# Optimization experiments

Hardware: AMD Instinct MI355X
Metric: run time of the kernel (lower is better)

## Reference

```python
import jax, jax.numpy as jnp
import numpy as np

B, DIN, DOUT, NW = 32768, 768, 768, 48
NH = NW // 3  # num_haar == num_mexican == num_morlet == 16 for NW=48
OMEGA0 = 5.0
LN_EPS = 1e-5


def setup_inputs() -> dict:
    key = jax.random.key(0)
    ks = jax.random.split(key, 6)
    x = jax.random.normal(ks[0], (B, DIN), dtype=jnp.float32)
    # kaiming-normal-ish fan_in init for linear layers, zero bias
    W = jax.random.normal(ks[1], (DOUT, DIN), dtype=jnp.float32) / np.sqrt(DIN)
    b = jnp.zeros((DOUT,), jnp.float32)
    Wp = jax.random.normal(ks[2], (NW, DIN), dtype=jnp.float32) / np.sqrt(DIN)
    bp = jnp.zeros((NW,), jnp.float32)
    Wc = jax.random.normal(ks[3], (DOUT, NW), dtype=jnp.float32) / np.sqrt(NW)
    bc = jnp.zeros((DOUT,), jnp.float32)
    # mixed-type init: per-family logspace scales / linspace translations
    scales = jnp.asarray(np.concatenate([
        np.logspace(-0.5, 0.5, NH),
        np.logspace(-0.3, 0.7, NH),
        np.logspace(-0.3, 0.7, NW - 2 * NH)]), jnp.float32)
    translations = jnp.asarray(np.concatenate([
        np.linspace(-1.5, 1.5, NH),
        np.linspace(-1.5, 1.5, NH),
        np.linspace(-1.5, 1.5, NW - 2 * NH)]), jnp.float32)
    gamma = jnp.ones((DOUT,), jnp.float32)
    beta = jnp.zeros((DOUT,), jnp.float32)
    return {"x": x, "W": W, "b": b, "Wp": Wp, "bp": bp, "Wc": Wc,
            "bc": bc, "scales": scales, "translations": translations,
            "gamma": gamma, "beta": beta}


def _wavelet_basis(s):
    # s: [B, NW] already scaled/translated; columns split by family
    dt = s.dtype
    sh = s[:, :NH]
    haar = (((sh >= 0) & (sh < 0.5)).astype(dt)
            - ((sh >= 0.5) & (sh < 1.0)).astype(dt))
    sm = s[:, NH:2 * NH]
    mexican = (1.0 - sm * sm) * jnp.exp(-0.5 * sm * sm)
    so = s[:, 2 * NH:]
    morlet = jnp.cos(OMEGA0 * so) * jnp.exp(-0.5 * so * so)
    return jnp.concatenate([haar, mexican, morlet], axis=1)


def reference(x, W, b, Wp, bp, Wc, bc, scales, translations, gamma, beta):
    direct = x @ W.T + b                              # [B, DOUT]
    wi = x @ Wp.T + bp                                # [B, NW]
    s = (wi - translations) / scales                  # [B, NW]
    wav = jax.nn.gelu(_wavelet_basis(s), approximate=False)
    wpath = wav @ Wc.T + bc                           # [B, DOUT]
    h = direct + wpath
    mu = jnp.mean(h, axis=-1, keepdims=True)
    var = jnp.mean((h - mu) ** 2, axis=-1, keepdims=True)
    return (h - mu) * jax.lax.rsqrt(var + LN_EPS) * gamma + beta
```

## Files before the change

### kernel.cpp

```cpp
#include <hip/hip_runtime.h>
#include <math.h>


#define B_SZ  32768
#define DIN   768
#define DOUT  768
#define NWAV  48

#define WF_OFF   0
#define WPH_OFF  589824
#define WPL_OFF  638976
#define WCF_OFF  688128

typedef short bf16x8 __attribute__((ext_vector_type(8)));
typedef float f32x16 __attribute__((ext_vector_type(16)));

__device__ __forceinline__ float bf2f(short u) {
    union { unsigned int i; float f; } v;
    v.i = ((unsigned int)(unsigned short)u) << 16;
    return v.f;
}
__device__ __forceinline__ short f2bf(float f) {
    union { float f; unsigned int i; } v; v.f = f;
    unsigned int r = v.i + 0x7FFFu + ((v.i >> 16) & 1u);
    return (short)(r >> 16);
}

__global__ __launch_bounds__(256) void pack_kernel(
    const float* __restrict__ W, const float* __restrict__ Wp,
    const float* __restrict__ Wc, short* __restrict__ ws)
{
    const int gw = (blockIdx.x * 256 + threadIdx.x) >> 6;
    const int L  = threadIdx.x & 63;
    const int lm = L & 31, half = L >> 5;

    if (gw < 1152) {
        const int cb = gw / 48, kb = gw % 48;
        const int row = cb * 32 + lm;
        const int k = kb * 16 + half * 8;
        bf16x8 o;
#pragma unroll
        for (int j = 0; j < 8; j++) o[j] = f2bf(W[(size_t)row * DIN + k + j]);
        *reinterpret_cast<bf16x8*>(&ws[WF_OFF + (size_t)gw * 512 + L * 8]) = o;
    } else if (gw < 1248) {
        const int t = gw - 1152;
        const int ct = t / 48, kb = t % 48;
        const int j = ct * 32 + lm;
        const int k = kb * 16 + half * 8;
        bf16x8 h, l;
#pragma unroll
        for (int jj = 0; jj < 8; jj++) {
            float v = (j < NWAV) ? Wp[(size_t)j * DIN + k + jj] : 0.f;
            const short hh = f2bf(v);
            h[jj] = hh;
            l[jj] = f2bf(v - bf2f(hh));
        }
        *reinterpret_cast<bf16x8*>(&ws[WPH_OFF + (size_t)t * 512 + L * 8]) = h;
        *reinterpret_cast<bf16x8*>(&ws[WPL_OFF + (size_t)t * 512 + L * 8]) = l;
    } else if (gw < 1320) {
        const int t = gw - 1248;
        const int cb = t / 3, kb = t % 3;
        const int row = cb * 32 + lm;
        const int k = kb * 16 + half * 8;
        bf16x8 o;
#pragma unroll
        for (int jj = 0; jj < 8; jj++) o[jj] = f2bf(Wc[(size_t)row * NWAV + k + jj]);
        *reinterpret_cast<bf16x8*>(&ws[WCF_OFF + (size_t)t * 512 + L * 8]) = o;
    }
}

__global__ __launch_bounds__(512, 2) void fused_kernel(
    const float* __restrict__ x, const short* __restrict__ ws,
    const float* __restrict__ Wp,
    const float* __restrict__ bp, const float* __restrict__ sc,
    const float* __restrict__ tr,
    const float* __restrict__ bb, const float* __restrict__ bc,
    const float* __restrict__ gm, const float* __restrict__ bt,
    float* __restrict__ out)
{
    __shared__ __align__(16) short xh[4][64 * 72];
    __shared__ __align__(16) short xl[4][64 * 72];
    __shared__ float redS[64 * 8], redQ[64 * 8];
    __shared__ float muA[64], rsA[64];
    __shared__ unsigned flags[64];
    __shared__ double dred[8];

    const short* WF  = ws + WF_OFF;
    const short* WPH = ws + WPH_OFF;
    const short* WPL = ws + WPL_OFF;
    const short* WCF = ws + WCF_OFF;

    const int tid = threadIdx.x;
    const int r0  = blockIdx.x * 64;
    const int L   = tid & 63;
    const int wv  = __builtin_amdgcn_readfirstlane(tid >> 6);
    const int lm  = L & 31, half = L >> 5;
    const int L8  = L * 8;
    const bool wi = (wv < 4);
    const int wv3 = wv * 3;
    const int wrt = wv & 1, wct = wv >> 1;
    const int wct48 = wct * 48;

    if (tid < 64) flags[tid] = 0u;

    f32x16 acc[2][3];
#pragma unroll
    for (int rt = 0; rt < 2; rt++)
#pragma unroll
        for (int ct = 0; ct < 3; ct++)
#pragma unroll
            for (int g = 0; g < 16; g++) acc[rt][ct][g] = 0.f;
    f32x16 wacc;
#pragma unroll
    for (int g = 0; g < 16; g++) wacc[g] = 0.f;

    const int srow = tid >> 3;
    const int sk   = (tid & 7) * 8;

#pragma unroll
    for (int c = 0; c < 2; ++c) {
        const float4* xp = reinterpret_cast<const float4*>(
            &x[(size_t)(r0 + srow) * DIN + c * 64 + sk]);
        const float4 v0 = xp[0], v1 = xp[1];
        const float f[8] = {v0.x, v0.y, v0.z, v0.w, v1.x, v1.y, v1.z, v1.w};
        bf16x8 hh, ll;
#pragma unroll
        for (int i = 0; i < 8; i++) {
            const short h = f2bf(f[i]);
            hh[i] = h;
            ll[i] = f2bf(f[i] - bf2f(h));
        }
        *reinterpret_cast<bf16x8*>(&xh[c][srow * 72 + sk]) = hh;
        *reinterpret_cast<bf16x8*>(&xl[c][srow * 72 + sk]) = ll;
    }
    __syncthreads();

    for (int s = 0; s < 6; ++s) {
        const int kA = 2 * s, kB = 2 * s + 1;
        const int bA = kA & 3, bB = kB & 3;
        const int kbA = kA * 4, kbB = kB * 4;

        bf16x8 bfrA[4][3];
#pragma unroll
        for (int ks = 0; ks < 4; ++ks)
#pragma unroll
            for (int ct = 0; ct < 3; ++ct)
                bfrA[ks][ct] = *reinterpret_cast<const bf16x8*>(
                    &WF[((size_t)((wv3 + ct) * 48 + kbA + ks)) * 512 + L8]);
        bf16x8 bwhA[4], bwlA[4];
        if (wi) {
#pragma unroll
            for (int ks = 0; ks < 4; ++ks) {
                bwhA[ks] = *reinterpret_cast<const bf16x8*>(
                    &WPH[((size_t)(wct48 + kbA + ks)) * 512 + L8]);
                bwlA[ks] = *reinterpret_cast<const bf16x8*>(
                    &WPL[((size_t)(wct48 + kbA + ks)) * 512 + L8]);
            }
        }
        float4 vA0, vA1;
        if (s < 5) {
            const float4* xp = reinterpret_cast<const float4*>(
                &x[(size_t)(r0 + srow) * DIN + (kA + 2) * 64 + sk]);
            vA0 = xp[0]; vA1 = xp[1];
        }

#pragma unroll
        for (int ks = 0; ks < 4; ++ks) {
            const bf16x8 a0 = *reinterpret_cast<bf16x8*>(
                &xh[bA][lm * 72 + ks * 16 + half * 8]);
            const bf16x8 a1 = *reinterpret_cast<bf16x8*>(
                &xh[bA][(32 + lm) * 72 + ks * 16 + half * 8]);
#pragma unroll
            for (int ct = 0; ct < 3; ++ct) {
                acc[0][ct] = __builtin_amdgcn_mfma_f32_32x32x16_bf16(a0, bfrA[ks][ct], acc[0][ct], 0, 0, 0);
                acc[1][ct] = __builtin_amdgcn_mfma_f32_32x32x16_bf16(a1, bfrA[ks][ct], acc[1][ct], 0, 0, 0);
            }
            if (wi) {
                const bf16x8 ah = wrt ? a1 : a0;
                const bf16x8 al = *reinterpret_cast<bf16x8*>(
                    &xl[bA][(wrt * 32 + lm) * 72 + ks * 16 + half * 8]);
                wacc = __builtin_amdgcn_mfma_f32_32x32x16_bf16(ah, bwlA[ks], wacc, 0, 0, 0);
                wacc = __builtin_amdgcn_mfma_f32_32x32x16_bf16(al, bwhA[ks], wacc, 0, 0, 0);
                wacc = __builtin_amdgcn_mfma_f32_32x32x16_bf16(ah, bwhA[ks], wacc, 0, 0, 0);
            }
        }

        bf16x8 bfrB[4][3];
#pragma unroll
        for (int ks = 0; ks < 4; ++ks)
#pragma unroll
            for (int ct = 0; ct < 3; ++ct)
                bfrB[ks][ct] = *reinterpret_cast<const bf16x8*>(
                    &WF[((size_t)((wv3 + ct) * 48 + kbB + ks)) * 512 + L8]);
        bf16x8 bwhB[4], bwlB[4];
        if (wi) {
#pragma unroll
            for (int ks = 0; ks < 4; ++ks) {
                bwhB[ks] = *reinterpret_cast<const bf16x8*>(
                    &WPH[((size_t)(wct48 + kbB + ks)) * 512 + L8]);
                bwlB[ks] = *reinterpret_cast<const bf16x8*>(
                    &WPL[((size_t)(wct48 + kbB + ks)) * 512 + L8]);
            }
        }
        float4 vB0, vB1;
        if (s < 5) {
            const float4* xp = reinterpret_cast<const float4*>(
                &x[(size_t)(r0 + srow) * DIN + (kB + 2) * 64 + sk]);
            vB0 = xp[0]; vB1 = xp[1];
        }

#pragma unroll
        for (int ks = 0; ks < 4; ++ks) {
            const bf16x8 a0 = *reinterpret_cast<bf16x8*>(
                &xh[bB][lm * 72 + ks * 16 + half * 8]);
            const bf16x8 a1 = *reinterpret_cast<bf16x8*>(
                &xh[bB][(32 + lm) * 72 + ks * 16 + half * 8]);
#pragma unroll
            for (int ct = 0; ct < 3; ++ct) {
                acc[0][ct] = __builtin_amdgcn_mfma_f32_32x32x16_bf16(a0, bfrB[ks][ct], acc[0][ct], 0, 0, 0);
                acc[1][ct] = __builtin_amdgcn_mfma_f32_32x32x16_bf16(a1, bfrB[ks][ct], acc[1][ct], 0, 0, 0);
            }
            if (wi) {
                const bf16x8 ah = wrt ? a1 : a0;
                const bf16x8 al = *reinterpret_cast<bf16x8*>(
                    &xl[bB][(wrt * 32 + lm) * 72 + ks * 16 + half * 8]);
                wacc = __builtin_amdgcn_mfma_f32_32x32x16_bf16(ah, bwlB[ks], wacc, 0, 0, 0);
                wacc = __builtin_amdgcn_mfma_f32_32x32x16_bf16(al, bwhB[ks], wacc, 0, 0, 0);
                wacc = __builtin_amdgcn_mfma_f32_32x32x16_bf16(ah, bwhB[ks], wacc, 0, 0, 0);
            }
        }

        if (s < 5) {
            {
                const float f[8] = {vA0.x, vA0.y, vA0.z, vA0.w, vA1.x, vA1.y, vA1.z, vA1.w};
                bf16x8 hh, ll;
#pragma unroll
                for (int i = 0; i < 8; i++) {
                    const short h = f2bf(f[i]);
                    hh[i] = h;
                    ll[i] = f2bf(f[i] - bf2f(h));
                }
                const int bn = (kA + 2) & 3;
                *reinterpret_cast<bf16x8*>(&xh[bn][srow * 72 + sk]) = hh;
                *reinterpret_cast<bf16x8*>(&xl[bn][srow * 72 + sk]) = ll;
            }
            {
                const float f[8] = {vB0.x, vB0.y, vB0.z, vB0.w, vB1.x, vB1.y, vB1.z, vB1.w};
                bf16x8 hh, ll;
#pragma unroll
                for (int i = 0; i < 8; i++) {
                    const short h = f2bf(f[i]);
                    hh[i] = h;
                    ll[i] = f2bf(f[i] - bf2f(h));
                }
                const int bn = (kB + 2) & 3;
                *reinterpret_cast<bf16x8*>(&xh[bn][srow * 72 + sk]) = hh;
                *reinterpret_cast<bf16x8*>(&xl[bn][srow * 72 + sk]) = ll;
            }
        }
        __syncthreads();
    }

    short* wavL = &xh[0][0];
    if (wi) {
        const int j = wct * 32 + lm;
        if (j < NWAV) {
            const float bpv = bp[j], scv = sc[j], trv = tr[j];
#pragma unroll
            for (int g = 0; g < 16; ++g) {
                const int rowl = wrt * 32 + (g & 3) + 8 * (g >> 2) + 4 * half;
                const float wiv = wacc[g] + bpv;
                const float s = (wiv - trv) / scv;
                float w;
                if (j < 16) {
                    const float dmin = fminf(fabsf(s), fminf(fabsf(s - 0.5f), fabsf(s - 1.0f)));
                    if (dmin < 2e-4f) atomicOr(&flags[rowl], 1u << j);
                    w = (s >= 0.f && s < 0.5f) ? 1.f : ((s >= 0.5f && s < 1.f) ? -1.f : 0.f);
                } else if (j < 32) {
                    w = (1.f - s * s) * expf(-0.5f * s * s);
                } else {
                    w = cosf(5.f * s) * expf(-0.5f * s * s);
                }
                const float gel = 0.5f * w * (1.f + erff(w * 0.70710678118654752f));
                wavL[rowl * 72 + j] = f2bf(gel);
            }
        }
    }
    __syncthreads();

#pragma unroll 1
    for (int fr = 0; fr < 64; ++fr) {
        unsigned m = flags[fr];
        while (m) {
            const int j = __ffs(m) - 1;
            m &= m - 1;
            const float* xr = &x[(size_t)(r0 + fr) * DIN];
            const float* wr = &Wp[(size_t)j * DIN];
            double a = (double)xr[tid] * (double)wr[tid];
            if (tid < DIN - 512)
                a += (double)xr[tid + 512] * (double)wr[tid + 512];
            a += __shfl_xor(a, 1);  a += __shfl_xor(a, 2);
            a += __shfl_xor(a, 4);  a += __shfl_xor(a, 8);
            a += __shfl_xor(a, 16); a += __shfl_xor(a, 32);
            if (L == 0) dred[wv] = a;
            __syncthreads();
            if (tid == 0) {
                double wid = (double)bp[j];
#pragma unroll
                for (int i = 0; i < 8; i++) wid += dred[i];
                const double sd = (wid - (double)tr[j]) / (double)sc[j];
                const double w = (sd >= 0.0 && sd < 0.5) ? 1.0
                               : ((sd >= 0.5 && sd < 1.0) ? -1.0 : 0.0);
                const double gel = 0.5 * w * (1.0 + erf(w * 0.70710678118654752));
                wavL[fr * 72 + j] = f2bf((float)gel);
            }
            __syncthreads();
        }
    }

#pragma unroll
    for (int ks = 0; ks < 3; ++ks) {
        const bf16x8 a0 = *reinterpret_cast<bf16x8*>(&wavL[lm * 72 + ks * 16 + half * 8]);
        const bf16x8 a1 = *reinterpret_cast<bf16x8*>(&wavL[(32 + lm) * 72 + ks * 16 + half * 8]);
#pragma unroll
        for (int ct = 0; ct < 3; ++ct) {
            const bf16x8 b = *reinterpret_cast<const bf16x8*>(
                &WCF[((size_t)((wv3 + ct) * 3 + ks)) * 512 + L8]);
            acc[0][ct] = __builtin_amdgcn_mfma_f32_32x32x16_bf16(a0, b, acc[0][ct], 0, 0, 0);
            acc[1][ct] = __builtin_amdgcn_mfma_f32_32x32x16_bf16(a1, b, acc[1][ct], 0, 0, 0);
        }
    }

    float bias[3], gmv[3], btv[3];
#pragma unroll
    for (int ct = 0; ct < 3; ++ct) {
        const int col = wv * 96 + ct * 32 + lm;
        bias[ct] = bb[col] + bc[col];
        gmv[ct] = gm[col];
        btv[ct] = bt[col];
    }
#pragma unroll
    for (int rt = 0; rt < 2; ++rt) {
#pragma unroll
        for (int g = 0; g < 16; ++g) {
            const float v0 = acc[rt][0][g] + bias[0];
            const float v1 = acc[rt][1][g] + bias[1];
            const float v2 = acc[rt][2][g] + bias[2];
            acc[rt][0][g] = v0; acc[rt][1][g] = v1; acc[rt][2][g] = v2;
            float s1 = v0 + v1 + v2;
            float s2 = v0 * v0 + v1 * v1 + v2 * v2;
            s1 += __shfl_xor(s1, 1);  s2 += __shfl_xor(s2, 1);
            s1 += __shfl_xor(s1, 2);  s2 += __shfl_xor(s2, 2);
            s1 += __shfl_xor(s1, 4);  s2 += __shfl_xor(s2, 4);
            s1 += __shfl_xor(s1, 8);  s2 += __shfl_xor(s2, 8);
            s1 += __shfl_xor(s1, 16); s2 += __shfl_xor(s2, 16);
            if (lm == 0) {
                const int rowl = rt * 32 + (g & 3) + 8 * (g >> 2) + 4 * half;
                redS[rowl * 8 + wv] = s1;
                redQ[rowl * 8 + wv] = s2;
            }
        }
    }
    __syncthreads();
    if (tid < 64) {
        float S = 0.f, Q = 0.f;
#pragma unroll
        for (int i = 0; i < 8; i++) { S += redS[tid * 8 + i]; Q += redQ[tid * 8 + i]; }
        const float mu = S * (1.f / 768.f);
        const float var = Q * (1.f / 768.f) - mu * mu;
        muA[tid] = mu;
        rsA[tid] = rsqrtf(var + 1e-5f);
    }
    __syncthreads();

#pragma unroll
    for (int rt = 0; rt < 2; ++rt) {
#pragma unroll
        for (int g = 0; g < 16; ++g) {
            const int rowl = rt * 32 + (g & 3) + 8 * (g >> 2) + 4 * half;
            const float mu = muA[rowl], rs = rsA[rowl];
            float* orow = &out[(size_t)(r0 + rowl) * DOUT + wv * 96 + lm];
#pragma unroll
            for (int ct = 0; ct < 3; ++ct) {
                orow[ct * 32] = (acc[rt][ct][g] - mu) * rs * gmv[ct] + btv[ct];
            }
        }
    }
}

extern "C" void kernel_launch(void* const* d_in, const int* in_sizes, int n_in,
                              void* d_out, int out_size, void* d_ws, size_t ws_size,
                              hipStream_t stream)
{
    const float* x  = (const float*)d_in[0];
    const float* W  = (const float*)d_in[1];
    const float* b  = (const float*)d_in[2];
    const float* Wp = (const float*)d_in[3];
    const float* bp = (const float*)d_in[4];
    const float* Wc = (const float*)d_in[5];
    const float* bc = (const float*)d_in[6];
    const float* sc = (const float*)d_in[7];
    const float* tr = (const float*)d_in[8];
    const float* gm = (const float*)d_in[9];
    const float* bt = (const float*)d_in[10];
    float* out = (float*)d_out;
    short* ws  = (short*)d_ws;

    pack_kernel<<<dim3(330), dim3(256), 0, stream>>>(W, Wp, Wc, ws);
    fused_kernel<<<dim3(B_SZ / 64), dim3(512), 0, stream>>>(
        x, ws, Wp, bp, sc, tr, b, bc, gm, bt, out);
}
```

Measured before the change: 265.9 us.

## Fuse weight packing into persistent main kernel with grid-wide barrier

Drops the separate pack kernel. The 256 blocks of the main kernel now pack the bf16 weight tiles themselves and wait on a global atomic-counter barrier before starting, and each block then handles two row tiles. The aim is to remove the second kernel launch and the serialization between the two kernels. The trade-offs are a hipMemsetAsync on every call, a spin barrier that deadlocks unless all 256 blocks are co-resident, and half as many blocks as before, which may reduce latency hiding.

```diff
diff --git a/kernel.cpp b/kernel.cpp
--- a/kernel.cpp
+++ b/kernel.cpp
@@ -11,6 +11,7 @@
 #define WPH_OFF  589824
 #define WPL_OFF  638976
 #define WCF_OFF  688128
+#define CTR_OFF  724992
 
 typedef short bf16x8 __attribute__((ext_vector_type(8)));
 typedef float f32x16 __attribute__((ext_vector_type(16)));
@@ -26,52 +27,10 @@
     return (short)(r >> 16);
 }
 
-__global__ __launch_bounds__(256) void pack_kernel(
-    const float* __restrict__ W, const float* __restrict__ Wp,
-    const float* __restrict__ Wc, short* __restrict__ ws)
-{
-    const int gw = (blockIdx.x * 256 + threadIdx.x) >> 6;
-    const int L  = threadIdx.x & 63;
-    const int lm = L & 31, half = L >> 5;
-
-    if (gw < 1152) {
-        const int cb = gw / 48, kb = gw % 48;
-        const int row = cb * 32 + lm;
-        const int k = kb * 16 + half * 8;
-        bf16x8 o;
-#pragma unroll
-        for (int j = 0; j < 8; j++) o[j] = f2bf(W[(size_t)row * DIN + k + j]);
-        *reinterpret_cast<bf16x8*>(&ws[WF_OFF + (size_t)gw * 512 + L * 8]) = o;
-    } else if (gw < 1248) {
-        const int t = gw - 1152;
-        const int ct = t / 48, kb = t % 48;
-        const int j = ct * 32 + lm;
-        const int k = kb * 16 + half * 8;
-        bf16x8 h, l;
-#pragma unroll
-        for (int jj = 0; jj < 8; jj++) {
-            float v = (j < NWAV) ? Wp[(size_t)j * DIN + k + jj] : 0.f;
-            const short hh = f2bf(v);
-            h[jj] = hh;
-            l[jj] = f2bf(v - bf2f(hh));
-        }
-        *reinterpret_cast<bf16x8*>(&ws[WPH_OFF + (size_t)t * 512 + L * 8]) = h;
-        *reinterpret_cast<bf16x8*>(&ws[WPL_OFF + (size_t)t * 512 + L * 8]) = l;
-    } else if (gw < 1320) {
-        const int t = gw - 1248;
-        const int cb = t / 3, kb = t % 3;
-        const int row = cb * 32 + lm;
-        const int k = kb * 16 + half * 8;
-        bf16x8 o;
-#pragma unroll
-        for (int jj = 0; jj < 8; jj++) o[jj] = f2bf(Wc[(size_t)row * NWAV + k + jj]);
-        *reinterpret_cast<bf16x8*>(&ws[WCF_OFF + (size_t)t * 512 + L * 8]) = o;
-    }
-}
-
 __global__ __launch_bounds__(512, 2) void fused_kernel(
-    const float* __restrict__ x, const short* __restrict__ ws,
-    const float* __restrict__ Wp,
+    const float* __restrict__ x,  const float* __restrict__ W,
+    const float* __restrict__ Wp, const float* __restrict__ Wc,
+    short* __restrict__ ws,
     const float* __restrict__ bp, const float* __restrict__ sc,
     const float* __restrict__ tr,
     const float* __restrict__ bb, const float* __restrict__ bc,
@@ -85,13 +44,7 @@
     __shared__ unsigned flags[64];
     __shared__ double dred[8];
 
-    const short* WF  = ws + WF_OFF;
-    const short* WPH = ws + WPH_OFF;
-    const short* WPL = ws + WPL_OFF;
-    const short* WCF = ws + WCF_OFF;
-
     const int tid = threadIdx.x;
-    const int r0  = blockIdx.x * 64;
     const int L   = tid & 63;
     const int wv  = __builtin_amdgcn_readfirstlane(tid >> 6);
     const int lm  = L & 31, half = L >> 5;
@@ -101,288 +54,347 @@
     const int wrt = wv & 1, wct = wv >> 1;
     const int wct48 = wct * 48;
 
-    if (tid < 64) flags[tid] = 0u;
-
-    f32x16 acc[2][3];
-#pragma unroll
-    for (int rt = 0; rt < 2; rt++)
-#pragma unroll
-        for (int ct = 0; ct < 3; ct++)
-#pragma unroll
-            for (int g = 0; g < 16; g++) acc[rt][ct][g] = 0.f;
-    f32x16 wacc;
-#pragma unroll
-    for (int g = 0; g < 16; g++) wacc[g] = 0.f;
+    {
+        const int gw = blockIdx.x * 8 + wv;
+        if (gw < 1152) {
+            const int cb = gw / 48, kb = gw % 48;
+            const int row = cb * 32 + lm;
+            const int k = kb * 16 + half * 8;
+            bf16x8 o;
+#pragma unroll
+            for (int j = 0; j < 8; j++) o[j] = f2bf(W[(size_t)row * DIN + k + j]);
+            *reinterpret_cast<bf16x8*>(&ws[WF_OFF + (size_t)gw * 512 + L8]) = o;
+        } else if (gw < 1248) {
+            const int t = gw - 1152;
+            const int ct = t / 48, kb = t % 48;
+            const int j = ct * 32 + lm;
+            const int k = kb * 16 + half * 8;
+            bf16x8 h, l;
+#pragma unroll
+            for (int jj = 0; jj < 8; jj++) {
+                float v = (j < NWAV) ? Wp[(size_t)j * DIN + k + jj] : 0.f;
+                const short hh = f2bf(v);
+                h[jj] = hh;
+                l[jj] = f2bf(v - bf2f(hh));
+            }
+            *reinterpret_cast<bf16x8*>(&ws[WPH_OFF + (size_t)t * 512 + L8]) = h;
+            *reinterpret_cast<bf16x8*>(&ws[WPL_OFF + (size_t)t * 512 + L8]) = l;
+        } else if (gw < 1320) {
+            const int t = gw - 1248;
+            const int cb = t / 3, kb = t % 3;
+            const int row = cb * 32 + lm;
+            const int k = kb * 16 + half * 8;
+            bf16x8 o;
+#pragma unroll
+            for (int jj = 0; jj < 8; jj++) o[jj] = f2bf(Wc[(size_t)row * NWAV + k + jj]);
+            *reinterpret_cast<bf16x8*>(&ws[WCF_OFF + (size_t)t * 512 + L8]) = o;
+        }
+    }
+
+    {
+        unsigned* ctr = reinterpret_cast<unsigned*>(ws + CTR_OFF);
+        __syncthreads();
+        if (tid == 0) {
+            __threadfence();
+            atomicAdd(ctr, 1u);
+            while (atomicAdd(ctr, 0u) < 256u) { }
+            __threadfence();
+        }
+        __syncthreads();
+    }
+
+    const short* WF  = ws + WF_OFF;
+    const short* WPH = ws + WPH_OFF;
+    const short* WPL = ws + WPL_OFF;
+    const short* WCF = ws + WCF_OFF;
 
     const int srow = tid >> 3;
     const int sk   = (tid & 7) * 8;
 
-#pragma unroll
-    for (int c = 0; c < 2; ++c) {
-        const float4* xp = reinterpret_cast<const float4*>(
-            &x[(size_t)(r0 + srow) * DIN + c * 64 + sk]);
-        const float4 v0 = xp[0], v1 = xp[1];
-        const float f[8] = {v0.x, v0.y, v0.z, v0.w, v1.x, v1.y, v1.z, v1.w};
-        bf16x8 hh, ll;
-#pragma unroll
-        for (int i = 0; i < 8; i++) {
-            const short h = f2bf(f[i]);
-            hh[i] = h;
-            ll[i] = f2bf(f[i] - bf2f(h));
-        }
-        *reinterpret_cast<bf16x8*>(&xh[c][srow * 72 + sk]) = hh;
-        *reinterpret_cast<bf16x8*>(&xl[c][srow * 72 + sk]) = ll;
-    }
-    __syncthreads();
-
-    for (int s = 0; s < 6; ++s) {
-        const int kA = 2 * s, kB = 2 * s + 1;
-        const int bA = kA & 3, bB = kB & 3;
-        const int kbA = kA * 4, kbB = kB * 4;
-
-        bf16x8 bfrA[4][3];
-#pragma unroll
-        for (int ks = 0; ks < 4; ++ks)
-#pragma unroll
-            for (int ct = 0; ct < 3; ++ct)
-                bfrA[ks][ct] = *reinterpret_cast<const bf16x8*>(
-                    &WF[((size_t)((wv3 + ct) * 48 + kbA + ks)) * 512 + L8]);
-        bf16x8 bwhA[4], bwlA[4];
+#pragma unroll 1
+    for (int pass = 0; pass < 2; ++pass) {
+        const int r0 = (blockIdx.x + (pass << 8)) * 64;
+
+        if (tid < 64) flags[tid] = 0u;
+
+        f32x16 acc[2][3];
+#pragma unroll
+        for (int rt = 0; rt < 2; rt++)
+#pragma unroll
+            for (int ct = 0; ct < 3; ct++)
+#pragma unroll
+                for (int g = 0; g < 16; g++) acc[rt][ct][g] = 0.f;
+        f32x16 wacc;
+#pragma unroll
+        for (int g = 0; g < 16; g++) wacc[g] = 0.f;
+
+#pragma unroll
+        for (int c = 0; c < 2; ++c) {
+            const float4* xp = reinterpret_cast<const float4*>(
+                &x[(size_t)(r0 + srow) * DIN + c * 64 + sk]);
+            const float4 v0 = xp[0], v1 = xp[1];
+            const float f[8] = {v0.x, v0.y, v0.z, v0.w, v1.x, v1.y, v1.z, v1.w};
+            bf16x8 hh, ll;
+#pragma unroll
+            for (int i = 0; i < 8; i++) {
+                const short h = f2bf(f[i]);
+                hh[i] = h;
+                ll[i] = f2bf(f[i] - bf2f(h));
+            }
+            *reinterpret_cast<bf16x8*>(&xh[c][srow * 72 + sk]) = hh;
+            *reinterpret_cast<bf16x8*>(&xl[c][srow * 72 + sk]) = ll;
+        }
+        __syncthreads();
+
+        for (int s = 0; s < 6; ++s) {
+            const int kA = 2 * s, kB = 2 * s + 1;
+            const int bA = kA & 3, bB = kB & 3;
+            const int kbA = kA * 4, kbB = kB * 4;
+
+            bf16x8 bfrA[4][3];
+#pragma unroll
+            for (int ks = 0; ks < 4; ++ks)
+#pragma unroll
+                for (int ct = 0; ct < 3; ++ct)
+                    bfrA[ks][ct] = *reinterpret_cast<const bf16x8*>(
+                        &WF[((size_t)((wv3 + ct) * 48 + kbA + ks)) * 512 + L8]);
+            bf16x8 bwhA[4], bwlA[4];
+            if (wi) {
+#pragma unroll
+                for (int ks = 0; ks < 4; ++ks) {
+                    bwhA[ks] = *reinterpret_cast<const bf16x8*>(
+                        &WPH[((size_t)(wct48 + kbA + ks)) * 512 + L8]);
+                    bwlA[ks] = *reinterpret_cast<const bf16x8*>(
+                        &WPL[((size_t)(wct48 + kbA + ks)) * 512 + L8]);
+                }
+            }
+            float4 vA0, vA1;
+            if (s < 5) {
+                const float4* xp = reinterpret_cast<const float4*>(
+                    &x[(size_t)(r0 + srow) * DIN + (kA + 2) * 64 + sk]);
+                vA0 = xp[0]; vA1 = xp[1];
+            }
+
+#pragma unroll
+            for (int ks = 0; ks < 4; ++ks) {
+                const bf16x8 a0 = *reinterpret_cast<bf16x8*>(
+                    &xh[bA][lm * 72 + ks * 16 + half * 8]);
+                const bf16x8 a1 = *reinterpret_cast<bf16x8*>(
+                    &xh[bA][(32 + lm) * 72 + ks * 16 + half * 8]);
+#pragma unroll
+                for (int ct = 0; ct < 3; ++ct) {
+                    acc[0][ct] = __builtin_amdgcn_mfma_f32_32x32x16_bf16(a0, bfrA[ks][ct], acc[0][ct], 0, 0, 0);
+                    acc[1][ct] = __builtin_amdgcn_mfma_f32_32x32x16_bf16(a1, bfrA[ks][ct], acc[1][ct], 0, 0, 0);
+                }
+                if (wi) {
+                    const bf16x8 ah = wrt ? a1 : a0;
+                    const bf16x8 al = *reinterpret_cast<bf16x8*>(
+                        &xl[bA][(wrt * 32 + lm) * 72 + ks * 16 + half * 8]);
+                    wacc = __builtin_amdgcn_mfma_f32_32x32x16_bf16(ah, bwlA[ks], wacc, 0, 0, 0);
+                    wacc = __builtin_amdgcn_mfma_f32_32x32x16_bf16(al, bwhA[ks], wacc, 0, 0, 0);
+                    wacc = __builtin_amdgcn_mfma_f32_32x32x16_bf16(ah, bwhA[ks], wacc, 0, 0, 0);
+                }
+            }
+
+            bf16x8 bfrB[4][3];
+#pragma unroll
+            for (int ks = 0; ks < 4; ++ks)
+#pragma unroll
+                for (int ct = 0; ct < 3; ++ct)
+                    bfrB[ks][ct] = *reinterpret_cast<const bf16x8*>(
+                        &WF[((size_t)((wv3 + ct) * 48 + kbB + ks)) * 512 + L8]);
+            bf16x8 bwhB[4], bwlB[4];
+            if (wi) {
+#pragma unroll
+                for (int ks = 0; ks < 4; ++ks) {
+                    bwhB[ks] = *reinterpret_cast<const bf16x8*>(
+                        &WPH[((size_t)(wct48 + kbB + ks)) * 512 + L8]);
+                    bwlB[ks] = *reinterpret_cast<const bf16x8*>(
+                        &WPL[((size_t)(wct48 + kbB + ks)) * 512 + L8]);
+                }
+            }
+            float4 vB0, vB1;
+            if (s < 5) {
+                const float4* xp = reinterpret_cast<const float4*>(
+                    &x[(size_t)(r0 + srow) * DIN + (kB + 2) * 64 + sk]);
+                vB0 = xp[0]; vB1 = xp[1];
+            }
+
+#pragma unroll
+            for (int ks = 0; ks < 4; ++ks) {
+                const bf16x8 a0 = *reinterpret_cast<bf16x8*>(
+                    &xh[bB][lm * 72 + ks * 16 + half * 8]);
+                const bf16x8 a1 = *reinterpret_cast<bf16x8*>(
+                    &xh[bB][(32 + lm) * 72 + ks * 16 + half * 8]);
+#pragma unroll
+                for (int ct = 0; ct < 3; ++ct) {
+                    acc[0][ct] = __builtin_amdgcn_mfma_f32_32x32x16_bf16(a0, bfrB[ks][ct], acc[0][ct], 0, 0, 0);
+                    acc[1][ct] = __builtin_amdgcn_mfma_f32_32x32x16_bf16(a1, bfrB[ks][ct], acc[1][ct], 0, 0, 0);
+                }
+                if (wi) {
+                    const bf16x8 ah = wrt ? a1 : a0;
+                    const bf16x8 al = *reinterpret_cast<bf16x8*>(
+                        &xl[bB][(wrt * 32 + lm) * 72 + ks * 16 + half * 8]);
+                    wacc = __builtin_amdgcn_mfma_f32_32x32x16_bf16(ah, bwlB[ks], wacc, 0, 0, 0);
+                    wacc = __builtin_amdgcn_mfma_f32_32x32x16_bf16(al, bwhB[ks], wacc, 0, 0, 0);
+                    wacc = __builtin_amdgcn_mfma_f32_32x32x16_bf16(ah, bwhB[ks], wacc, 0, 0, 0);
+                }
+            }
+
+            if (s < 5) {
+                {
+                    const float f[8] = {vA0.x, vA0.y, vA0.z, vA0.w, vA1.x, vA1.y, vA1.z, vA1.w};
+                    bf16x8 hh, ll;
+#pragma unroll
+                    for (int i = 0; i < 8; i++) {
+                        const short h = f2bf(f[i]);
+                        hh[i] = h;
+                        ll[i] = f2bf(f[i] - bf2f(h));
+                    }
+                    const int bn = (kA + 2) & 3;
+                    *reinterpret_cast<bf16x8*>(&xh[bn][srow * 72 + sk]) = hh;
+                    *reinterpret_cast<bf16x8*>(&xl[bn][srow * 72 + sk]) = ll;
+                }
+                {
+                    const float f[8] = {vB0.x, vB0.y, vB0.z, vB0.w, vB1.x, vB1.y, vB1.z, vB1.w};
+                    bf16x8 hh, ll;
+#pragma unroll
+                    for (int i = 0; i < 8; i++) {
+                        const short h = f2bf(f[i]);
+                        hh[i] = h;
+                        ll[i] = f2bf(f[i] - bf2f(h));
+                    }
+                    const int bn = (kB + 2) & 3;
+                    *reinterpret_cast<bf16x8*>(&xh[bn][srow * 72 + sk]) = hh;
+                    *reinterpret_cast<bf16x8*>(&xl[bn][srow * 72 + sk]) = ll;
+                }
+            }
+            __syncthreads();
+        }
+
+        short* wavL = &xh[0][0];
         if (wi) {
-#pragma unroll
-            for (int ks = 0; ks < 4; ++ks) {
-                bwhA[ks] = *reinterpret_cast<const bf16x8*>(
-                    &WPH[((size_t)(wct48 + kbA + ks)) * 512 + L8]);
-                bwlA[ks] = *reinterpret_cast<const bf16x8*>(
-                    &WPL[((size_t)(wct48 + kbA + ks)) * 512 + L8]);
-            }
-        }
-        float4 vA0, vA1;
-        if (s < 5) {
-            const float4* xp = reinterpret_cast<const float4*>(
-                &x[(size_t)(r0 + srow) * DIN + (kA + 2) * 64 + sk]);
-            vA0 = xp[0]; vA1 = xp[1];
-        }
-
-#pragma unroll
-        for (int ks = 0; ks < 4; ++ks) {
-            const bf16x8 a0 = *reinterpret_cast<bf16x8*>(
-                &xh[bA][lm * 72 + ks * 16 + half * 8]);
-            const bf16x8 a1 = *reinterpret_cast<bf16x8*>(
-                &xh[bA][(32 + lm) * 72 + ks * 16 + half * 8]);
+            const int j = wct * 32 + lm;
+            if (j < NWAV) {
+                const float bpv = bp[j], scv = sc[j], trv = tr[j];
+#pragma unroll
+                for (int g = 0; g < 16; ++g) {
+                    const int rowl = wrt * 32 + (g & 3) + 8 * (g >> 2) + 4 * half;
+                    const float wiv = wacc[g] + bpv;
+                    const float s = (wiv - trv) / scv;
+                    float w;
+                    if (j < 16) {
+                        const float dmin = fminf(fabsf(s), fminf(fabsf(s - 0.5f), fabsf(s - 1.0f)));
+                        if (dmin < 2e-4f) atomicOr(&flags[rowl], 1u << j);
+                        w = (s >= 0.f && s < 0.5f) ? 1.f : ((s >= 0.5f && s < 1.f) ? -1.f : 0.f);
+                    } else if (j < 32) {
+                        w = (1.f - s * s) * expf(-0.5f * s * s);
+                    } else {
+                        w = cosf(5.f * s) * expf(-0.5f * s * s);
+                    }
+                    const float gel = 0.5f * w * (1.f + erff(w * 0.70710678118654752f));
+                    wavL[rowl * 72 + j] = f2bf(gel);
+                }
+            }
+        }
+        __syncthreads();
+
+#pragma unroll 1
+        for (int fr = 0; fr < 64; ++fr) {
+            unsigned m = flags[fr];
+            while (m) {
+                const int j = __ffs(m) - 1;
+                m &= m - 1;
+                const float* xr = &x[(size_t)(r0 + fr) * DIN];
+                const float* wr = &Wp[(size_t)j * DIN];
+                double a = (double)xr[tid] * (double)wr[tid];
+                if (tid < DIN - 512)
+                    a += (double)xr[tid + 512] * (double)wr[tid + 512];
+                a += __shfl_xor(a, 1);  a += __shfl_xor(a, 2);
+                a += __shfl_xor(a, 4);  a += __shfl_xor(a, 8);
+                a += __shfl_xor(a, 16); a += __shfl_xor(a, 32);
+                if (L == 0) dred[wv] = a;
+                __syncthreads();
+                if (tid == 0) {
+                    double wid = (double)bp[j];
+#pragma unroll
+                    for (int i = 0; i < 8; i++) wid += dred[i];
+                    const double sd = (wid - (double)tr[j]) / (double)sc[j];
+                    const double w = (sd >= 0.0 && sd < 0.5) ? 1.0
+                                   : ((sd >= 0.5 && sd < 1.0) ? -1.0 : 0.0);
+                    const double gel = 0.5 * w * (1.0 + erf(w * 0.70710678118654752));
+                    wavL[fr * 72 + j] = f2bf((float)gel);
+                }
+                __syncthreads();
+            }
+        }
+
+#pragma unroll
+        for (int ks = 0; ks < 3; ++ks) {
+            const bf16x8 a0 = *reinterpret_cast<bf16x8*>(&wavL[lm * 72 + ks * 16 + half * 8]);
+            const bf16x8 a1 = *reinterpret_cast<bf16x8*>(&wavL[(32 + lm) * 72 + ks * 16 + half * 8]);
 #pragma unroll
             for (int ct = 0; ct < 3; ++ct) {
-                acc[0][ct] = __builtin_amdgcn_mfma_f32_32x32x16_bf16(a0, bfrA[ks][ct], acc[0][ct], 0, 0, 0);
-                acc[1][ct] = __builtin_amdgcn_mfma_f32_32x32x16_bf16(a1, bfrA[ks][ct], acc[1][ct], 0, 0, 0);
-            }
-            if (wi) {
-                const bf16x8 ah = wrt ? a1 : a0;
-                const bf16x8 al = *reinterpret_cast<bf16x8*>(
-                    &xl[bA][(wrt * 32 + lm) * 72 + ks * 16 + half * 8]);
-                wacc = __builtin_amdgcn_mfma_f32_32x32x16_bf16(ah, bwlA[ks], wacc, 0, 0, 0);
-                wacc = __builtin_amdgcn_mfma_f32_32x32x16_bf16(al, bwhA[ks], wacc, 0, 0, 0);
-                wacc = __builtin_amdgcn_mfma_f32_32x32x16_bf16(ah, bwhA[ks], wacc, 0, 0, 0);
-            }
-        }
-
-        bf16x8 bfrB[4][3];
-#pragma unroll
-        for (int ks = 0; ks < 4; ++ks)
-#pragma unroll
-            for (int ct = 0; ct < 3; ++ct)
-                bfrB[ks][ct] = *reinterpret_cast<const bf16x8*>(
-                    &WF[((size_t)((wv3 + ct) * 48 + kbB + ks)) * 512 + L8]);
-        bf16x8 bwhB[4], bwlB[4];
-        if (wi) {
-#pragma unroll
-            for (int ks = 0; ks < 4; ++ks) {
-                bwhB[ks] = *reinterpret_cast<const bf16x8*>(
-                    &WPH[((size_t)(wct48 + kbB + ks)) * 512 + L8]);
-                bwlB[ks] = *reinterpret_cast<const bf16x8*>(
-                    &WPL[((size_t)(wct48 + kbB + ks)) * 512 + L8]);
-            }
-        }
-        float4 vB0, vB1;
-        if (s < 5) {
-            const float4* xp = reinterpret_cast<const float4*>(
-                &x[(size_t)(r0 + srow) * DIN + (kB + 2) * 64 + sk]);
-            vB0 = xp[0]; vB1 = xp[1];
-        }
-
-#pragma unroll
-        for (int ks = 0; ks < 4; ++ks) {
-            const bf16x8 a0 = *reinterpret_cast<bf16x8*>(
-                &xh[bB][lm * 72 + ks * 16 + half * 8]);
-            const bf16x8 a1 = *reinterpret_cast<bf16x8*>(
-                &xh[bB][(32 + lm) * 72 + ks * 16 + half * 8]);
-#pragma unroll
-            for (int ct = 0; ct < 3; ++ct) {
-                acc[0][ct] = __builtin_amdgcn_mfma_f32_32x32x16_bf16(a0, bfrB[ks][ct], acc[0][ct], 0, 0, 0);
-                acc[1][ct] = __builtin_amdgcn_mfma_f32_32x32x16_bf16(a1, bfrB[ks][ct], acc[1][ct], 0, 0, 0);
-            }
-            if (wi) {
-                const bf16x8 ah = wrt ? a1 : a0;
-                const bf16x8 al = *reinterpret_cast<bf16x8*>(
-                    &xl[bB][(wrt * 32 + lm) * 72 + ks * 16 + half * 8]);
-                wacc = __builtin_amdgcn_mfma_f32_32x32x16_bf16(ah, bwlB[ks], wacc, 0, 0, 0);
-                wacc = __builtin_amdgcn_mfma_f32_32x32x16_bf16(al, bwhB[ks], wacc, 0, 0, 0);
-                wacc = __builtin_amdgcn_mfma_f32_32x32x16_bf16(ah, bwhB[ks], wacc, 0, 0, 0);
-            }
-        }
-
-        if (s < 5) {
-            {
-                const float f[8] = {vA0.x, vA0.y, vA0.z, vA0.w, vA1.x, vA1.y, vA1.z, vA1.w};
-                bf16x8 hh, ll;
-#pragma unroll
-                for (int i = 0; i < 8; i++) {
-                    const short h = f2bf(f[i]);
-                    hh[i] = h;
-                    ll[i] = f2bf(f[i] - bf2f(h));
-                }
-                const int bn = (kA + 2) & 3;
-                *reinterpret_cast<bf16x8*>(&xh[bn][srow * 72 + sk]) = hh;
-                *reinterpret_cast<bf16x8*>(&xl[bn][srow * 72 + sk]) = ll;
-            }
-            {
-                const float f[8] = {vB0.x, vB0.y, vB0.z, vB0.w, vB1.x, vB1.y, vB1.z, vB1.w};
-                bf16x8 hh, ll;
-#pragma unroll
-                for (int i = 0; i < 8; i++) {
-                    const short h = f2bf(f[i]);
-                    hh[i] = h;
-                    ll[i] = f2bf(f[i] - bf2f(h));
-                }
-                const int bn = (kB + 2) & 3;
-                *reinterpret_cast<bf16x8*>(&xh[bn][srow * 72 + sk]) = hh;
-                *reinterpret_cast<bf16x8*>(&xl[bn][srow * 72 + sk]) = ll;
-            }
-        }
-        __syncthreads();
-    }
-
-    short* wavL = &xh[0][0];
-    if (wi) {
-        const int j = wct * 32 + lm;
-        if (j < NWAV) {
-            const float bpv = bp[j], scv = sc[j], trv = tr[j];
+                const bf16x8 b = *reinterpret_cast<const bf16x8*>(
+                    &WCF[((size_t)((wv3 + ct) * 3 + ks)) * 512 + L8]);
+                acc[0][ct] = __builtin_amdgcn_mfma_f32_32x32x16_bf16(a0, b, acc[0][ct], 0, 0, 0);
+                acc[1][ct] = __builtin_amdgcn_mfma_f32_32x32x16_bf16(a1, b, acc[1][ct], 0, 0, 0);
+            }
+        }
+
+        float bias[3], gmv[3], btv[3];
+#pragma unroll
+        for (int ct = 0; ct < 3; ++ct) {
+            const int col = wv * 96 + ct * 32 + lm;
+            bias[ct] = bb[col] + bc[col];
+            gmv[ct] = gm[col];
+            btv[ct] = bt[col];
+        }
+#pragma unroll
+        for (int rt = 0; rt < 2; ++rt) {
 #pragma unroll
             for (int g = 0; g < 16; ++g) {
-                const int rowl = wrt * 32 + (g & 3) + 8 * (g >> 2) + 4 * half;
-                const float wiv = wacc[g] + bpv;
-                const float s = (wiv - trv) / scv;
-                float w;
-                if (j < 16) {
-                    const float dmin = fminf(fabsf(s), fminf(fabsf(s - 0.5f), fabsf(s - 1.0f)));
-                    if (dmin < 2e-4f) atomicOr(&flags[rowl], 1u << j);
-                    w = (s >= 0.f && s < 0.5f) ? 1.f : ((s >= 0.5f && s < 1.f) ? -1.f : 0.f);
-                } else if (j < 32) {
-                    w = (1.f - s * s) * expf(-0.5f * s * s);
-                } else {
-                    w = cosf(5.f * s) * expf(-0.5f * s * s);
-                }
-                const float gel = 0.5f * w * (1.f + erff(w * 0.70710678118654752f));
-                wavL[rowl * 72 + j] = f2bf(gel);
-            }
-        }
-    }
-    __syncthreads();
-
-#pragma unroll 1
-    for (int fr = 0; fr < 64; ++fr) {
-        unsigned m = flags[fr];
-        while (m) {
-            const int j = __ffs(m) - 1;
-            m &= m - 1;
-            const float* xr = &x[(size_t)(r0 + fr) * DIN];
-            const float* wr = &Wp[(size_t)j * DIN];
-            double a = (double)xr[tid] * (double)wr[tid];
-            if (tid < DIN - 512)
-                a += (double)xr[tid + 512] * (double)wr[tid + 512];
-            a += __shfl_xor(a, 1);  a += __shfl_xor(a, 2);
-            a += __shfl_xor(a, 4);  a += __shfl_xor(a, 8);
-            a += __shfl_xor(a, 16); a += __shfl_xor(a, 32);
-            if (L == 0) dred[wv] = a;
-            __syncthreads();
-            if (tid == 0) {
-                double wid = (double)bp[j];
-#pragma unroll
-                for (int i = 0; i < 8; i++) wid += dred[i];
-                const double sd = (wid - (double)tr[j]) / (double)sc[j];
-                const double w = (sd >= 0.0 && sd < 0.5) ? 1.0
-                               : ((sd >= 0.5 && sd < 1.0) ? -1.0 : 0.0);
-                const double gel = 0.5 * w * (1.0 + erf(w * 0.70710678118654752));
-                wavL[fr * 72 + j] = f2bf((float)gel);
-            }
-            __syncthreads();
-        }
-    }
-
-#pragma unroll
-    for (int ks = 0; ks < 3; ++ks) {
-        const bf16x8 a0 = *reinterpret_cast<bf16x8*>(&wavL[lm * 72 + ks * 16 + half * 8]);
-        const bf16x8 a1 = *reinterpret_cast<bf16x8*>(&wavL[(32 + lm) * 72 + ks * 16 + half * 8]);
-#pragma unroll
-        for (int ct = 0; ct < 3; ++ct) {
-            const bf16x8 b = *reinterpret_cast<const bf16x8*>(
-                &WCF[((size_t)((wv3 + ct) * 3 + ks)) * 512 + L8]);
-            acc[0][ct] = __builtin_amdgcn_mfma_f32_32x32x16_bf16(a0, b, acc[0][ct], 0, 0, 0);
-            acc[1][ct] = __builtin_amdgcn_mfma_f32_32x32x16_bf16(a1, b, acc[1][ct], 0, 0, 0);
-        }
-    }
-
-    float bias[3], gmv[3], btv[3];
-#pragma unroll
-    for (int ct = 0; ct < 3; ++ct) {
-        const int col = wv * 96 + ct * 32 + lm;
-        bias[ct] = bb[col] + bc[col];
-        gmv[ct] = gm[col];
-        btv[ct] = bt[col];
-    }
-#pragma unroll
-    for (int rt = 0; rt < 2; ++rt) {
-#pragma unroll
-        for (int g = 0; g < 16; ++g) {
-            const float v0 = acc[rt][0][g] + bias[0];
-            const float v1 = acc[rt][1][g] + bias[1];
-            const float v2 = acc[rt][2][g] + bias[2];
-            acc[rt][0][g] = v0; acc[rt][1][g] = v1; acc[rt][2][g] = v2;
-            float s1 = v0 + v1 + v2;
-            float s2 = v0 * v0 + v1 * v1 + v2 * v2;
-            s1 += __shfl_xor(s1, 1);  s2 += __shfl_xor(s2, 1);
-            s1 += __shfl_xor(s1, 2);  s2 += __shfl_xor(s2, 2);
-            s1 += __shfl_xor(s1, 4);  s2 += __shfl_xor(s2, 4);
-            s1 += __shfl_xor(s1, 8);  s2 += __shfl_xor(s2, 8);
-            s1 += __shfl_xor(s1, 16); s2 += __shfl_xor(s2, 16);
-            if (lm == 0) {
+                const float v0 = acc[rt][0][g] + bias[0];
+                const float v1 = acc[rt][1][g] + bias[1];
+                const float v2 = acc[rt][2][g] + bias[2];
+                acc[rt][0][g] = v0; acc[rt][1][g] = v1; acc[rt][2][g] = v2;
+                float s1 = v0 + v1 + v2;
+                float s2 = v0 * v0 + v1 * v1 + v2 * v2;
+                s1 += __shfl_xor(s1, 1);  s2 += __shfl_xor(s2, 1);
+                s1 += __shfl_xor(s1, 2);  s2 += __shfl_xor(s2, 2);
+                s1 += __shfl_xor(s1, 4);  s2 += __shfl_xor(s2, 4);
+                s1 += __shfl_xor(s1, 8);  s2 += __shfl_xor(s2, 8);
+                s1 += __shfl_xor(s1, 16); s2 += __shfl_xor(s2, 16);
+                if (lm == 0) {
+                    const int rowl = rt * 32 + (g & 3) + 8 * (g >> 2) + 4 * half;
+                    redS[rowl * 8 + wv] = s1;
+                    redQ[rowl * 8 + wv] = s2;
+                }
+            }
+        }
+        __syncthreads();
+        if (tid < 64) {
+            float S = 0.f, Q = 0.f;
+#pragma unroll
+            for (int i = 0; i < 8; i++) { S += redS[tid * 8 + i]; Q += redQ[tid * 8 + i]; }
+            const float mu = S * (1.f / 768.f);
+            const float var = Q * (1.f / 768.f) - mu * mu;
+            muA[tid] = mu;
+            rsA[tid] = rsqrtf(var + 1e-5f);
+        }
+        __syncthreads();
+
+#pragma unroll
+        for (int rt = 0; rt < 2; ++rt) {
+#pragma unroll
+            for (int g = 0; g < 16; ++g) {
                 const int rowl = rt * 32 + (g & 3) + 8 * (g >> 2) + 4 * half;
-                redS[rowl * 8 + wv] = s1;
-                redQ[rowl * 8 + wv] = s2;
-            }
-        }
-    }
-    __syncthreads();
-    if (tid < 64) {
-        float S = 0.f, Q = 0.f;
-#pragma unroll
-        for (int i = 0; i < 8; i++) { S += redS[tid * 8 + i]; Q += redQ[tid * 8 + i]; }
-        const float mu = S * (1.f / 768.f);
-        const float var = Q * (1.f / 768.f) - mu * mu;
-        muA[tid] = mu;
-        rsA[tid] = rsqrtf(var + 1e-5f);
-    }
-    __syncthreads();
-
-#pragma unroll
-    for (int rt = 0; rt < 2; ++rt) {
-#pragma unroll
-        for (int g = 0; g < 16; ++g) {
-            const int rowl = rt * 32 + (g & 3) + 8 * (g >> 2) + 4 * half;
-            const float mu = muA[rowl], rs = rsA[rowl];
-            float* orow = &out[(size_t)(r0 + rowl) * DOUT + wv * 96 + lm];
-#pragma unroll
-            for (int ct = 0; ct < 3; ++ct) {
-                orow[ct * 32] = (acc[rt][ct][g] - mu) * rs * gmv[ct] + btv[ct];
+                const float mu = muA[rowl], rs = rsA[rowl];
+                float* orow = &out[(size_t)(r0 + rowl) * DOUT + wv * 96 + lm];
+#pragma unroll
+                for (int ct = 0; ct < 3; ++ct) {
+                    orow[ct * 32] = (acc[rt][ct][g] - mu) * rs * gmv[ct] + btv[ct];
+                }
             }
         }
     }
@@ -406,7 +418,7 @@
     float* out = (float*)d_out;
     short* ws  = (short*)d_ws;
 
-    pack_kernel<<<dim3(330), dim3(256), 0, stream>>>(W, Wp, Wc, ws);
-    fused_kernel<<<dim3(B_SZ / 64), dim3(512), 0, stream>>>(
-        x, ws, Wp, bp, sc, tr, b, bc, gm, bt, out);
+    hipMemsetAsync(ws + CTR_OFF, 0, 4, stream);
+    fused_kernel<<<dim3(256), dim3(512), 0, stream>>>(
+        x, W, Wp, Wc, ws, bp, sc, tr, b, bc, gm, bt, out);
 }
```

Result: slower. 393.3 us (+47.9%).
